# Performance work log

Measured on AMD Instinct MI355X. Metric: run time of the kernel, lower is better.

Reference implementation:

```python
import jax, jax.numpy as jnp
import numpy as np

N_FFT = 512
HOP = 128
WIN = 512
Q = 0.1
PCT_WIN = 31
FREQ_WIN = 5
TIME_WIN = 9
STRENGTH = 0.35
THRESH = 1.5
TEMP = 0.15
MIN_MASK = 0.08


def _hann_periodic(n):
    # matches torch.hann_window(n) (periodic)
    return (0.5 * (1.0 - jnp.cos(2.0 * jnp.pi * jnp.arange(n) / n))).astype(jnp.float32)


def _stft(x, window):
    # x: (B, L) -> complex (B, F, T); center=True, reflect pad
    pad = N_FFT // 2
    xp = jnp.pad(x, ((0, 0), (pad, pad)), mode='reflect')
    T = 1 + (xp.shape[-1] - N_FFT) // HOP
    idx = (jnp.arange(T) * HOP)[:, None] + jnp.arange(N_FFT)  # (T, n_fft)
    frames = xp[:, idx] * window  # (B, T, n_fft)
    return jnp.fft.rfft(frames, axis=-1).transpose(0, 2, 1)  # (B, F, T)


def _istft(spec, window, length):
    # spec: (B, F, T) complex -> (B, length)
    frames = jnp.fft.irfft(spec.transpose(0, 2, 1), n=N_FFT, axis=-1) * window  # (B,T,n_fft)
    B, T, _ = frames.shape
    total = N_FFT + HOP * (T - 1)
    idx = ((jnp.arange(T) * HOP)[:, None] + jnp.arange(N_FFT)).ravel()
    out = jnp.zeros((B, total), frames.dtype).at[:, idx].add(frames.reshape(B, -1))
    wsq = jnp.zeros((total,), frames.dtype).at[idx].add(
        jnp.broadcast_to(window ** 2, (T, N_FFT)).ravel())
    out = out / jnp.maximum(wsq, 1e-11)
    pad = N_FFT // 2
    return out[:, pad:pad + length]


def _rolling_quantile(mag):
    # mag: (B, F, T); replicate pad + sliding window of PCT_WIN along time
    p = PCT_WIN // 2
    padded = jnp.pad(mag, ((0, 0), (0, 0), (p, p)), mode='edge')
    T = mag.shape[-1]
    windows = jnp.stack([padded[..., i:i + T] for i in range(PCT_WIN)], axis=-1)  # (B,F,T,W)
    return jnp.quantile(windows, Q, axis=-1)


def _avg_pool(x, k, axis):
    # stride-1 avg pool with zero pad k//2, count_include_pad=True (torch default)
    if k <= 1:
        return x
    p = k // 2
    pads = [(0, 0)] * x.ndim
    pads[axis] = (p, p)
    xp = jnp.pad(x, pads)
    n = x.shape[axis]
    acc = 0.0
    for i in range(k):
        sl = [slice(None)] * x.ndim
        sl[axis] = slice(i, i + n)
        acc = acc + xp[tuple(sl)]
    return acc / k


def setup_inputs() -> dict:
    key = jax.random.key(0)
    k1, k2 = jax.random.split(key)
    B, L = 16, 160000
    noisy = jax.random.normal(k1, (B, L), dtype=jnp.float32)
    enhanced = jax.random.normal(k2, (B, L), dtype=jnp.float32)
    return {"noisy": noisy, "enhanced": enhanced}


def reference(noisy, enhanced):
    length = enhanced.shape[-1]
    window = _hann_periodic(WIN)
    e_spec = _stft(enhanced, window)
    n_spec = _stft(noisy, window)
    e_mag = jnp.maximum(jnp.abs(e_spec), 1e-6)
    n_mag = jnp.maximum(jnp.abs(n_spec), 1e-6)
    # mode == 'sg_input_floor': source is the noisy magnitude
    floor = _rolling_quantile(n_mag)
    floor = _avg_pool(floor, FREQ_WIN, axis=-2)
    floor = _avg_pool(floor, TIME_WIN, axis=-1)
    floor = jnp.maximum(floor, 1e-6)
    mask = jax.nn.sigmoid((e_mag - THRESH * floor) / (TEMP * floor + 1e-6))
    final_mask = MIN_MASK + (1.0 - MIN_MASK) * (1.0 - STRENGTH + STRENGTH * mask)
    phase = e_spec / jnp.maximum(jnp.abs(e_spec), 1e-12)  # unit-phase, = polar(1, angle)
    gated_spec = (e_mag * final_mask).astype(jnp.float32) * phase
    return _istft(gated_spec, window, length)
```

## Files before the change

### kernel.cpp

```cpp
#include <hip/hip_runtime.h>
#include <hip/hip_bf16.h>
#include <math.h>

#define BATCH 16
#define LEN   160000
#define NFFT  512
#define HOP   128
#define NT    1251
#define NF    257
#define PADC  256
#define TWO_PI 6.28318530717958647692f
#define P(i) ((i) + ((i) >> 5))
#define FBUF 528
#define GSTR 264

typedef unsigned int u32;
typedef unsigned short u16t;

__device__ __forceinline__ float rcpf(float x)  { return __builtin_amdgcn_rcpf(x); }
__device__ __forceinline__ float sqrtf_fast(float x) { return __builtin_amdgcn_sqrtf(x); }

__device__ __forceinline__ int reflect_idx(int j) {
    j = j < 0 ? -j : j;
    j = j >= LEN ? 2*LEN - 2 - j : j;
    return j;
}

__device__ __forceinline__ float hann(int n) {
    return 0.5f - 0.5f * __cosf(TWO_PI * (float)n * (1.0f / 512.0f));
}

__device__ __forceinline__ void hann8(int j, float wdv[8]) {
    float sth, cth;
    __sincosf((TWO_PI / 512.0f) * (float)j, &sth, &cth);
    const float K8 = 0.70710678118654752f;
    const float A = 0.5f * K8 * (cth - sth);
    const float B = 0.5f * K8 * (cth + sth);
    wdv[0] = 0.5f - 0.5f * cth;
    wdv[1] = 0.5f - A;
    wdv[2] = 0.5f + 0.5f * sth;
    wdv[3] = 0.5f + B;
    wdv[4] = 0.5f + 0.5f * cth;
    wdv[5] = 0.5f + A;
    wdv[6] = 0.5f - 0.5f * sth;
    wdv[7] = 0.5f - B;
}

__device__ __forceinline__ __hip_bfloat162 pack_bf2(float x, float y) {
    __hip_bfloat162 r; r.x = __float2bfloat16(x); r.y = __float2bfloat16(y); return r;
}
__device__ __forceinline__ float2 unpack_bf2(__hip_bfloat162 v) {
    return make_float2(__bfloat162float(v.x), __bfloat162float(v.y));
}

struct T4 { float m0, m1, m2, m3; };

__device__ __forceinline__ void ins(T4& a, float v) {
    const float x0 = fminf(a.m0, v);  const float c0 = fmaxf(a.m0, v);
    const float x1 = fminf(a.m1, c0); const float c1 = fmaxf(a.m1, c0);
    const float x2 = fminf(a.m2, c1); const float c2 = fmaxf(a.m2, c1);
    const float x3 = fminf(a.m3, c2);
    a.m0 = x0; a.m1 = x1; a.m2 = x2; a.m3 = x3;
}

__device__ __forceinline__ u32 pminP(u32 a, u32 b) {
    u32 d; asm("v_pk_min_u16 %0, %1, %2" : "=v"(d) : "v"(a), "v"(b)); return d;
}
__device__ __forceinline__ u32 pmaxP(u32 a, u32 b) {
    u32 d; asm("v_pk_max_u16 %0, %1, %2" : "=v"(d) : "v"(a), "v"(b)); return d;
}

struct PT4 { u32 m0, m1, m2, m3; };

__device__ __forceinline__ void insP(PT4& a, u32 v) {
    const u32 x0 = pminP(a.m0, v);  const u32 c0 = pmaxP(a.m0, v);
    const u32 x1 = pminP(a.m1, c0); const u32 c1 = pmaxP(a.m1, c0);
    const u32 x2 = pminP(a.m2, c1); const u32 c2 = pmaxP(a.m2, c1);
    const u32 x3 = pminP(a.m3, c2);
    a.m0 = x0; a.m1 = x1; a.m2 = x2; a.m3 = x3;
}

__device__ __forceinline__ PT4 sort4P(u32 a, u32 b, u32 c, u32 d) {
    const u32 x0 = pminP(a, b), x1 = pmaxP(a, b);
    const u32 x2 = pminP(c, d), x3 = pmaxP(c, d);
    const u32 y0 = pminP(x0, x2), y2 = pmaxP(x0, x2);
    const u32 y1 = pminP(x1, x3), y3 = pmaxP(x1, x3);
    PT4 r; r.m0 = y0; r.m1 = pminP(y1, y2); r.m2 = pmaxP(y1, y2); r.m3 = y3;
    return r;
}

__device__ __forceinline__ u32 merge4_m3P(const PT4& a, const PT4& b) {
    const u32 l0 = pminP(a.m0, b.m3);
    const u32 l1 = pminP(a.m1, b.m2);
    const u32 l2 = pminP(a.m2, b.m1);
    const u32 l3 = pminP(a.m3, b.m0);
    return pmaxP(pmaxP(l0, l1), pmaxP(l2, l3));
}

__device__ __forceinline__ void dft8(float vr[8], float vi[8], float sign) {
    const float K = 0.70710678118654752f;
    float ar=vr[0]+vr[4], ai=vi[0]+vi[4];
    float br=vr[0]-vr[4], bi=vi[0]-vi[4];
    float cr=vr[2]+vr[6], ci=vi[2]+vi[6];
    float dr=vr[2]-vr[6], di=vi[2]-vi[6];
    float er=vr[1]+vr[5], ei=vi[1]+vi[5];
    float fr=vr[1]-vr[5], fi=vi[1]-vi[5];
    float gr=vr[3]+vr[7], gi=vi[3]+vi[7];
    float hr=vr[3]-vr[7], hi=vi[3]-vi[7];
    const float W4dr = -sign*di, W4di = sign*dr;
    const float W4hr = -sign*hi, W4hi = sign*hr;
    const float E0r=ar+cr, E0i=ai+ci, E2r=ar-cr, E2i=ai-ci;
    const float E1r=br+W4dr, E1i=bi+W4di, E3r=br-W4dr, E3i=bi-W4di;
    const float O0r=er+gr, O0i=ei+gi, O2r=er-gr, O2i=ei-gi;
    const float O1r=fr+W4hr, O1i=fi+W4hi, O3r=fr-W4hr, O3i=fi-W4hi;
    const float T1r = K*(O1r - sign*O1i), T1i = K*(O1i + sign*O1r);
    const float T2r = -sign*O2i,          T2i = sign*O2r;
    const float T3r = K*(-O3r - sign*O3i), T3i = K*(-O3i + sign*O3r);
    vr[0]=E0r+O0r; vi[0]=E0i+O0i;  vr[4]=E0r-O0r; vi[4]=E0i-O0i;
    vr[1]=E1r+T1r; vi[1]=E1i+T1i;  vr[5]=E1r-T1r; vi[5]=E1i-T1i;
    vr[2]=E2r+T2r; vi[2]=E2i+T2i;  vr[6]=E2r-T2r; vi[6]=E2i-T2i;
    vr[3]=E3r+T3r; vi[3]=E3i+T3i;  vr[7]=E3r-T3r; vi[7]=E3i-T3i;
}

template<int NS>
__device__ __forceinline__ void fft_pass(float* R, float* I, int j, float sign) {
    float vr[8], vi[8];
    #pragma unroll
    for (int r = 0; r < 8; ++r) { vr[r] = R[P(j + 64*r)]; vi[r] = I[P(j + 64*r)]; }
    const float th = sign * (TWO_PI / (8.0f * (float)NS)) * (float)(j & (NS - 1));
    float w1r, w1i; __sincosf(th, &w1i, &w1r);
    float wr = w1r, wi = w1i;
    #pragma unroll
    for (int r = 1; r < 8; ++r) {
        const float tr = vr[r]*wr - vi[r]*wi;
        vi[r] = vr[r]*wi + vi[r]*wr; vr[r] = tr;
        const float nwr = wr*w1r - wi*w1i;
        wi = wr*w1i + wi*w1r; wr = nwr;
    }
    dft8(vr, vi, sign);
    const int base = ((j / NS) * (8 * NS)) + (j & (NS - 1));
    #pragma unroll
    for (int r = 0; r < 8; ++r) { R[P(base + r*NS)] = vr[r]; I[P(base + r*NS)] = vi[r]; }
}

__device__ __forceinline__ void fft_pass_last(const float* R, const float* I, int j,
                                              float sign, float vr[8], float vi[8]) {
    #pragma unroll
    for (int r = 0; r < 8; ++r) { vr[r] = R[P(j + 64*r)]; vi[r] = I[P(j + 64*r)]; }
    const float th = sign * (TWO_PI / 512.0f) * (float)j;
    float w1r, w1i; __sincosf(th, &w1i, &w1r);
    float wr = w1r, wi = w1i;
    #pragma unroll
    for (int r = 1; r < 8; ++r) {
        const float tr = vr[r]*wr - vi[r]*wi;
        vi[r] = vr[r]*wi + vi[r]*wr; vr[r] = tr;
        const float nwr = wr*w1r - wi*w1i;
        wi = wr*w1i + wi*w1r; wr = nwr;
    }
    dft8(vr, vi, sign);
}

__global__ __launch_bounds__(256, 6) void stft_kernel(const float* __restrict__ enh,
                                                      const float* __restrict__ noi,
                                                      __hip_bfloat162* __restrict__ e_spec,
                                                      __hip_bfloat16*  __restrict__ n_mag,
                                                      float* __restrict__ out) {
    __shared__ float Ar[4*FBUF], Ai[4*FBUF];
    const int tid = threadIdx.x;
    const int w = tid >> 6, j = tid & 63;
    const int tr_ = blockIdx.x * 4 + w;
    const bool live = tr_ < NT;
    const int t = live ? tr_ : NT - 1;
    const int b = blockIdx.y;
    float* ar = Ar + w*FBUF; float* ai = Ai + w*FBUF;

    {
        const int z = (blockIdx.x << 9) + (tid << 1);
        if (z < LEN) *reinterpret_cast<float2*>(out + (size_t)b * LEN + z) = make_float2(0.0f, 0.0f);
    }

    {
        const int sbase = t * HOP - PADC;
        float vr[8], vi[8];
        if (sbase >= 0 && sbase + NFFT <= LEN) {
            const float* __restrict__ pe = enh + b * LEN + sbase;
            const float* __restrict__ pn = noi + b * LEN + sbase;
            float wdv[8];
            hann8(j, wdv);
            #pragma unroll
            for (int r = 0; r < 8; ++r) {
                const int n = j + 64*r;
                vr[r] = pe[n] * wdv[r];
                vi[r] = pn[n] * wdv[r];
            }
        } else {
            const float* __restrict__ pe = enh + b * LEN;
            const float* __restrict__ pn = noi + b * LEN;
            #pragma unroll
            for (int r = 0; r < 8; ++r) {
                const int n = j + 64*r;
                const int idx = reflect_idx(sbase + n);
                const float wd = hann(n);
                vr[r] = pe[idx] * wd;
                vi[r] = pn[idx] * wd;
            }
        }
        dft8(vr, vi, -1.0f);
        #pragma unroll
        for (int r = 0; r < 8; ++r) { ar[P(8*j + r)] = vr[r]; ai[P(8*j + r)] = vi[r]; }
    }
    fft_pass<8>(ar, ai, j, -1.0f);
    float zr[8], zi[8];
    fft_pass_last(ar, ai, j, -1.0f, zr, zi);

    const int src = (64 - j) & 63;
    float pr[4], pi_[4];
    #pragma unroll
    for (int q = 4; q < 8; ++q) {
        pr[q-4]  = __shfl(zr[q], src);
        pi_[q-4] = __shfl(zi[q], src);
    }
    if (live) {
        const int obase = (b * NT + t) * NF;
        #pragma unroll
        for (int r = 0; r < 4; ++r) {
            const int kk = j + 64*r;
            const float yr = (j == 0) ? zr[(8 - r) & 7] : pr[3 - r];
            const float yi = (j == 0) ? zi[(8 - r) & 7] : pi_[3 - r];
            const float er = 0.5f*(zr[r] + yr), ei = 0.5f*(zi[r] - yi);
            const float nr = 0.5f*(zi[r] + yi), ni = 0.5f*(yr - zr[r]);
            e_spec[obase + kk] = pack_bf2(er, ei);
            n_mag[obase + kk] = __float2bfloat16(fmaxf(sqrtf_fast(nr*nr + ni*ni), 1e-6f));
        }
        if (j == 0) {
            e_spec[obase + 256] = pack_bf2(zr[4], 0.0f);
            n_mag[obase + 256] = __float2bfloat16(fmaxf(fabsf(zi[4]), 1e-6f));
        }
    }
}

template<bool CL>
__device__ __forceinline__ void phaseQP(const u16t* __restrict__ pbu,
                                        int t0, int f, float qv[16]) {
    u16t wlo[16];
    #pragma unroll
    for (int r = 0; r < 16; ++r) {
        int tr = t0 - 19 + r;
        if (CL) { tr = tr < 0 ? 0 : (tr > NT - 1 ? NT - 1 : tr); }
        wlo[r] = pbu[tr * NF + f];
    }
    PT4 S[8];
    S[7].m0 = (u32)wlo[7] | ((u32)wlo[15] << 16);
    S[7].m1 = S[7].m2 = S[7].m3 = 0xFFFFFFFFu;
    #pragma unroll
    for (int k = 6; k >= 0; --k) {
        S[k] = S[k+1];
        insP(S[k], (u32)wlo[k] | ((u32)wlo[k+8] << 16));
    }
    u16t ring[8];
    #pragma unroll
    for (int i = 0; i < 8; ++i) ring[i] = wlo[8 + i];
    PT4 Pp;
    {
        u32 Wt[4];
        #pragma unroll
        for (int r = 8; r < 12; ++r) {
            int tr = t0 - 19 + r + 8;
            if (CL) { tr = tr < 0 ? 0 : (tr > NT - 1 ? NT - 1 : tr); }
            const u16t hi = pbu[tr * NF + f];
            Wt[r - 8] = (u32)ring[r & 7] | ((u32)hi << 16);
            ring[r & 7] = hi;
        }
        Pp = sort4P(Wt[0], Wt[1], Wt[2], Wt[3]);
    }
    #pragma unroll
    for (int r = 12; r < 31; ++r) {
        int tr = t0 - 19 + r + 8;
        if (CL) { tr = tr < 0 ? 0 : (tr > NT - 1 ? NT - 1 : tr); }
        const u16t hi = pbu[tr * NF + f];
        insP(Pp, (u32)ring[r & 7] | ((u32)hi << 16));
        ring[r & 7] = hi;
    }
    {
        const u32 m = merge4_m3P(S[0], Pp);
        qv[0] = __uint_as_float(m << 16);
        qv[8] = __uint_as_float(m & 0xFFFF0000u);
    }
    #pragma unroll
    for (int k = 1; k < 8; ++k) {
        const int r = 30 + k;
        int tr = t0 - 19 + r + 8;
        if (CL) { tr = tr < 0 ? 0 : (tr > NT - 1 ? NT - 1 : tr); }
        const u16t hi = pbu[tr * NF + f];
        insP(Pp, (u32)ring[r & 7] | ((u32)hi << 16));
        ring[r & 7] = hi;
        const u32 m = merge4_m3P(S[k], Pp);
        qv[k]     = __uint_as_float(m << 16);
        qv[8 + k] = __uint_as_float(m & 0xFFFF0000u);
    }
}

__global__ __launch_bounds__(256, 4) void floor_mask_istft_kernel(
        const __hip_bfloat162* __restrict__ g,
        const __hip_bfloat16* __restrict__ n_mag,
        float* __restrict__ out) {
    __shared__ float smem[16 * GSTR];
    float* TPl = smem;
    float* gr = smem;
    float* gi = smem + 8 * GSTR;

    const int tid = threadIdx.x;
    const int w = tid >> 6, j = tid & 63;
    const int t0 = blockIdx.x * 8, b = blockIdx.y;
    const __hip_bfloat16* __restrict__ pb = n_mag + b * NT * NF;
    const u16t* __restrict__ pbu = (const u16t*)pb;
    const int f = tid;

    float qv[16];
    if (t0 >= 19 && t0 + 26 <= NT - 1) {
        phaseQP<false>(pbu, t0, f, qv);
    } else {
        phaseQP<true>(pbu, t0, f, qv);
        #pragma unroll
        for (int k = 0; k < 16; ++k) {
            const int tq = t0 - 4 + k;
            if (tq < 0 || tq >= NT) qv[k] = 0.0f;
        }
    }
    {
        float acc = 0.0f;
        #pragma unroll
        for (int k = 0; k < 9; ++k) acc += qv[k];
        #pragma unroll
        for (int to = 0; to < 8; ++to) {
            TPl[to * GSTR + f] = acc * (1.0f / 9.0f);
            if (to < 7) acc += qv[to + 9] - qv[to];
        }
    }
    if (tid < 16) {
        const int k = tid;
        T4 m; m.m0 = m.m1 = m.m2 = m.m3 = 3.4e38f;
        for (int dt = -15; dt <= 15; ++dt) {
            int tt = t0 - 4 + k + dt;
            tt = tt < 0 ? 0 : (tt > NT - 1 ? NT - 1 : tt);
            ins(m, __bfloat162float(pb[tt * NF + 256]));
        }
        float qk = m.m3;
        const int tq = t0 - 4 + k;
        if (tq < 0 || tq >= NT) qk = 0.0f;
        float acc = 0.0f;
        #pragma unroll
        for (int d = 0; d < 9; ++d) acc += __shfl(qk, k + d);
        if (tid < 8) TPl[tid * GSTR + 256] = acc * (1.0f / 9.0f);
    }
    __syncthreads();

    float fl[8];
    #pragma unroll
    for (int to = 0; to < 8; ++to) {
        float acc = 0.0f;
        #pragma unroll
        for (int df = -2; df <= 2; ++df) {
            const int ff = f + df;
            if (ff >= 0 && ff < NF) acc += TPl[to * GSTR + ff];
        }
        fl[to] = fmaxf(acc * (1.0f / 5.0f), 1e-6f);
    }
    float fl256 = 0.0f;
    if (tid < 8) {
        fl256 = fmaxf((TPl[tid * GSTR + 254] + TPl[tid * GSTR + 255] +
                       TPl[tid * GSTR + 256]) * (1.0f / 5.0f), 1e-6f);
    }
    __syncthreads();

    {
        #pragma unroll
        for (int ft = 0; ft < 8; ++ft) {
            const int t = t0 + ft;
            float grv = 0.0f, giv = 0.0f;
            if (t < NT) {
                const float flv = fl[ft];
                const float2 e2 = unpack_bf2(g[(b * NT + t) * NF + f]);
                const float a = sqrtf_fast(e2.x * e2.x + e2.y * e2.y);
                const float emag = fmaxf(a, 1e-6f);
                const float xarg = (emag - 1.5f * flv) * rcpf(0.15f * flv + 1e-6f);
                const float mask = rcpf(1.0f + __expf(-xarg));
                const float fm = 0.08f + 0.92f * (0.65f + 0.35f * mask);
                const float scale = emag * fm * rcpf(fmaxf(a, 1e-12f));
                grv = e2.x * scale; giv = e2.y * scale;
            }
            gr[ft * GSTR + f] = grv;
            gi[ft * GSTR + f] = giv;
        }
    }
    if (tid < 8) {
        const int ft = tid;
        const int t = t0 + ft;
        float grv = 0.0f, giv = 0.0f;
        if (t < NT) {
            const float flv = fl256;
            const float2 e2 = unpack_bf2(g[(b * NT + t) * NF + 256]);
            const float a = sqrtf_fast(e2.x * e2.x + e2.y * e2.y);
            const float emag = fmaxf(a, 1e-6f);
            const float xarg = (emag - 1.5f * flv) * rcpf(0.15f * flv + 1e-6f);
            const float mask = rcpf(1.0f + __expf(-xarg));
            const float fm = 0.08f + 0.92f * (0.65f + 0.35f * mask);
            const float scale = emag * fm * rcpf(fmaxf(a, 1e-12f));
            grv = e2.x * scale; giv = e2.y * scale;
        }
        gr[ft * GSTR + 256] = grv;
        gi[ft * GSTR + 256] = giv;
    }
    __syncthreads();

    float* g0r = gr + (2*w) * GSTR;      float* g0i = gi + (2*w) * GSTR;
    float* g1r = gr + (2*w + 1) * GSTR;  float* g1i = gi + (2*w + 1) * GSTR;
    float* ar = g0r;
    float* ai = g0i;

    {
        float vr[8], vi[8];
        #pragma unroll
        for (int r = 0; r < 8; ++r) {
            const int n = j + 64*r;
            float cr, ci;
            if (n <= 256) {
                cr = g0r[n] - g1i[n];
                ci = g0i[n] + g1r[n];
            } else {
                const int m = 512 - n;
                cr = g0r[m] + g1i[m];
                ci = g1r[m] - g0i[m];
            }
            vr[r] = cr; vi[r] = ci;
        }
        dft8(vr, vi, 1.0f);
        #pragma unroll
        for (int r = 0; r < 8; ++r) { ar[P(8*j + r)] = vr[r]; ai[P(8*j + r)] = vi[r]; }
    }
    fft_pass<8>(ar, ai, j, 1.0f);
    float xr[8], xi[8];
    fft_pass_last(ar, ai, j, 1.0f, xr, xi);

    {
        float wdv[8];
        hann8(j, wdv);
        #pragma unroll
        for (int r = 0; r < 8; ++r) {
            const int n = j + 64*r;
            const float wd = wdv[r] * (1.0f / 512.0f);
            ar[P(n)] = xr[r] * wd;
            ai[P(n)] = xi[r] * wd;
        }
    }
    __syncthreads();

    const int i0 = t0 << 7;
    if (t0 >= 3 && t0 + 10 <= NT - 1) {
        for (int s = tid; s < 1408; s += 256) {
            const int i = i0 + s;
            const int tl = (i - 384) >> 7;
            const int th = tl + 3;
            const int ca = tl > t0 ? tl : t0;
            const int cb = th < t0 + 7 ? th : t0 + 7;
            float acc = 0.0f;
            for (int t = ca; t <= cb; ++t) {
                const int ft = t - t0;
                const int n = i - (t << 7);
                acc += ((ft & 1) ? gi : gr)[(ft >> 1) * FBUF + P(n)];
            }
            const float v = acc * (2.0f / 3.0f);
            const int jj = i - PADC;
            if (tl >= t0 && th <= t0 + 7) out[b * LEN + jj] = v;
            else atomicAdd(out + b * LEN + jj, v);
        }
    } else {
        for (int s = tid; s < 1408; s += 256) {
            const int i = i0 + s;
            const int jj = i - PADC;
            if (jj < 0 || jj >= LEN) continue;
            const int tl = (i >= 384) ? ((i - 384) >> 7) : 0;
            int th = i >> 7; if (th > NT - 1) th = NT - 1;
            const int ca = tl > t0 ? tl : t0;
            const int cb = th < t0 + 7 ? th : t0 + 7;
            if (cb < ca) continue;
            float acc = 0.0f;
            for (int t = ca; t <= cb; ++t) {
                const int ft = t - t0;
                const int n = i - (t << 7);
                acc += ((ft & 1) ? gi : gr)[(ft >> 1) * FBUF + P(n)];
            }
            float winv;
            if (th - tl == 3) winv = (2.0f / 3.0f);
            else {
                float wacc = 0.0f;
                for (int t = tl; t <= th; ++t) {
                    const float wd = hann(i - (t << 7));
                    wacc += wd * wd;
                }
                winv = rcpf(fmaxf(wacc, 1e-11f));
            }
            const float v = acc * winv;
            if (tl >= t0 && th <= t0 + 7) out[b * LEN + jj] = v;
            else atomicAdd(out + b * LEN + jj, v);
        }
    }
}

extern "C" void kernel_launch(void* const* d_in, const int* in_sizes, int n_in,
                              void* d_out, int out_size, void* d_ws, size_t ws_size,
                              hipStream_t stream) {
    const float* noisy    = (const float*)d_in[0];
    const float* enhanced = (const float*)d_in[1];
    float* out = (float*)d_out;

    float* ws = (float*)d_ws;
    __hip_bfloat162* e_spec = (__hip_bfloat162*)ws;
    __hip_bfloat16* n_mag = (__hip_bfloat16*)(ws + 5144112);

    stft_kernel<<<dim3((NT + 3) / 4, BATCH), dim3(256), 0, stream>>>(enhanced, noisy, e_spec, n_mag, out);
    floor_mask_istft_kernel<<<dim3((NT + 7) / 8, BATCH), dim3(256), 0, stream>>>(e_spec, n_mag, out);
}
```

Measured before the change: 122.3 us.

## Widen floor/mask/iSTFT kernel to 16 frames per block with 512 threads

The fused floor/mask/iSTFT kernel now handles 16 time frames per block instead of 8, using 512 threads split into two halves. Each half computes 12 rolling-quantile values into shared memory, and the time-pool then reads them back. This amortizes the 31-wide quantile window halo and the iSTFT overlap edges (fewer atomicAdds) across more frames. In exchange it uses more shared memory per block, adds an extra barrier, and runs fewer, larger blocks, which changes occupancy.

```diff
diff --git a/kernel.cpp b/kernel.cpp
--- a/kernel.cpp
+++ b/kernel.cpp
@@ -240,104 +240,100 @@
 }
 
 template<bool CL>
-__device__ __forceinline__ void phaseQP(const u16t* __restrict__ pbu,
-                                        int t0, int f, float qv[16]) {
-    u16t wlo[16];
-    #pragma unroll
-    for (int r = 0; r < 16; ++r) {
-        int tr = t0 - 19 + r;
+__device__ __forceinline__ void phaseQ12(const u16t* __restrict__ pbu,
+                                         int base, int f, float qv[12]) {
+    u16t w0[12];
+    #pragma unroll
+    for (int r = 0; r < 12; ++r) {
+        int tr = base + r;
         if (CL) { tr = tr < 0 ? 0 : (tr > NT - 1 ? NT - 1 : tr); }
-        wlo[r] = pbu[tr * NF + f];
-    }
-    PT4 S[8];
-    S[7].m0 = (u32)wlo[7] | ((u32)wlo[15] << 16);
-    S[7].m1 = S[7].m2 = S[7].m3 = 0xFFFFFFFFu;
-    #pragma unroll
-    for (int k = 6; k >= 0; --k) {
+        w0[r] = pbu[tr * NF + f];
+    }
+    PT4 S[6];
+    S[5].m0 = (u32)w0[5] | ((u32)w0[11] << 16);
+    S[5].m1 = S[5].m2 = S[5].m3 = 0xFFFFFFFFu;
+    #pragma unroll
+    for (int k = 4; k >= 0; --k) {
         S[k] = S[k+1];
-        insP(S[k], (u32)wlo[k] | ((u32)wlo[k+8] << 16));
-    }
-    u16t ring[8];
-    #pragma unroll
-    for (int i = 0; i < 8; ++i) ring[i] = wlo[8 + i];
+        insP(S[k], (u32)w0[k] | ((u32)w0[k+6] << 16));
+    }
+    u16t ring[6];
+    #pragma unroll
+    for (int i = 0; i < 6; ++i) ring[i] = w0[6 + i];
     PT4 Pp;
     {
         u32 Wt[4];
         #pragma unroll
-        for (int r = 8; r < 12; ++r) {
-            int tr = t0 - 19 + r + 8;
+        for (int r = 6; r < 10; ++r) {
+            int tr = base + r + 6;
             if (CL) { tr = tr < 0 ? 0 : (tr > NT - 1 ? NT - 1 : tr); }
             const u16t hi = pbu[tr * NF + f];
-            Wt[r - 8] = (u32)ring[r & 7] | ((u32)hi << 16);
-            ring[r & 7] = hi;
+            Wt[r - 6] = (u32)ring[r % 6] | ((u32)hi << 16);
+            ring[r % 6] = hi;
         }
         Pp = sort4P(Wt[0], Wt[1], Wt[2], Wt[3]);
     }
     #pragma unroll
-    for (int r = 12; r < 31; ++r) {
-        int tr = t0 - 19 + r + 8;
+    for (int r = 10; r < 31; ++r) {
+        int tr = base + r + 6;
         if (CL) { tr = tr < 0 ? 0 : (tr > NT - 1 ? NT - 1 : tr); }
         const u16t hi = pbu[tr * NF + f];
-        insP(Pp, (u32)ring[r & 7] | ((u32)hi << 16));
-        ring[r & 7] = hi;
+        insP(Pp, (u32)ring[r % 6] | ((u32)hi << 16));
+        ring[r % 6] = hi;
     }
     {
         const u32 m = merge4_m3P(S[0], Pp);
         qv[0] = __uint_as_float(m << 16);
-        qv[8] = __uint_as_float(m & 0xFFFF0000u);
-    }
-    #pragma unroll
-    for (int k = 1; k < 8; ++k) {
+        qv[6] = __uint_as_float(m & 0xFFFF0000u);
+    }
+    #pragma unroll
+    for (int k = 1; k < 6; ++k) {
         const int r = 30 + k;
-        int tr = t0 - 19 + r + 8;
+        int tr = base + r + 6;
         if (CL) { tr = tr < 0 ? 0 : (tr > NT - 1 ? NT - 1 : tr); }
         const u16t hi = pbu[tr * NF + f];
-        insP(Pp, (u32)ring[r & 7] | ((u32)hi << 16));
-        ring[r & 7] = hi;
+        insP(Pp, (u32)ring[r % 6] | ((u32)hi << 16));
+        ring[r % 6] = hi;
         const u32 m = merge4_m3P(S[k], Pp);
         qv[k]     = __uint_as_float(m << 16);
-        qv[8 + k] = __uint_as_float(m & 0xFFFF0000u);
-    }
-}
-
-__global__ __launch_bounds__(256, 4) void floor_mask_istft_kernel(
+        qv[6 + k] = __uint_as_float(m & 0xFFFF0000u);
+    }
+}
+
+__global__ __launch_bounds__(512, 6) void floor_mask_istft_kernel(
         const __hip_bfloat162* __restrict__ g,
         const __hip_bfloat16* __restrict__ n_mag,
         float* __restrict__ out) {
-    __shared__ float smem[16 * GSTR];
-    float* TPl = smem;
+    __shared__ float smem[40 * GSTR];
+    float (*q)[GSTR] = reinterpret_cast<float (*)[GSTR]>(smem);
+    float* TPl = smem + 24 * GSTR;
     float* gr = smem;
-    float* gi = smem + 8 * GSTR;
+    float* gi = smem + 16 * GSTR;
 
     const int tid = threadIdx.x;
     const int w = tid >> 6, j = tid & 63;
-    const int t0 = blockIdx.x * 8, b = blockIdx.y;
+    const int h = tid >> 8, f = tid & 255;
+    const int t0 = blockIdx.x * 16, b = blockIdx.y;
     const __hip_bfloat16* __restrict__ pb = n_mag + b * NT * NF;
     const u16t* __restrict__ pbu = (const u16t*)pb;
-    const int f = tid;
-
-    float qv[16];
-    if (t0 >= 19 && t0 + 26 <= NT - 1) {
-        phaseQP<false>(pbu, t0, f, qv);
-    } else {
-        phaseQP<true>(pbu, t0, f, qv);
-        #pragma unroll
-        for (int k = 0; k < 16; ++k) {
-            const int tq = t0 - 4 + k;
-            if (tq < 0 || tq >= NT) qv[k] = 0.0f;
-        }
-    }
-    {
-        float acc = 0.0f;
-        #pragma unroll
-        for (int k = 0; k < 9; ++k) acc += qv[k];
-        #pragma unroll
-        for (int to = 0; to < 8; ++to) {
-            TPl[to * GSTR + f] = acc * (1.0f / 9.0f);
-            if (to < 7) acc += qv[to + 9] - qv[to];
-        }
-    }
-    if (tid < 16) {
+
+    {
+        float qv[12];
+        const int base = t0 - 19 + 12 * h;
+        if (t0 >= 19 && t0 + 34 <= NT - 1) {
+            phaseQ12<false>(pbu, base, f, qv);
+        } else {
+            phaseQ12<true>(pbu, base, f, qv);
+            #pragma unroll
+            for (int i = 0; i < 12; ++i) {
+                const int tq = t0 - 4 + 12 * h + i;
+                if (tq < 0 || tq >= NT) qv[i] = 0.0f;
+            }
+        }
+        #pragma unroll
+        for (int i = 0; i < 12; ++i) q[12 * h + i][f] = qv[i];
+    }
+    if (tid < 24) {
         const int k = tid;
         T4 m; m.m0 = m.m1 = m.m2 = m.m3 = 3.4e38f;
         for (int dt = -15; dt <= 15; ++dt) {
@@ -348,26 +344,45 @@
         float qk = m.m3;
         const int tq = t0 - 4 + k;
         if (tq < 0 || tq >= NT) qk = 0.0f;
+        q[k][256] = qk;
+    }
+    __syncthreads();
+
+    {
+        float qr[16];
+        #pragma unroll
+        for (int i = 0; i < 16; ++i) qr[i] = q[8 * h + i][f];
         float acc = 0.0f;
         #pragma unroll
-        for (int d = 0; d < 9; ++d) acc += __shfl(qk, k + d);
-        if (tid < 8) TPl[tid * GSTR + 256] = acc * (1.0f / 9.0f);
+        for (int i = 0; i < 9; ++i) acc += qr[i];
+        #pragma unroll
+        for (int ft_ = 0; ft_ < 8; ++ft_) {
+            TPl[(8 * h + ft_) * GSTR + f] = acc * (1.0f / 9.0f);
+            if (ft_ < 7) acc += qr[ft_ + 9] - qr[ft_];
+        }
+    }
+    if (tid < 16) {
+        float acc = 0.0f;
+        #pragma unroll
+        for (int d = 0; d < 9; ++d) acc += q[tid + d][256];
+        TPl[tid * GSTR + 256] = acc * (1.0f / 9.0f);
     }
     __syncthreads();
 
     float fl[8];
     #pragma unroll
-    for (int to = 0; to < 8; ++to) {
+    for (int ft_ = 0; ft_ < 8; ++ft_) {
+        const int row = 8 * h + ft_;
         float acc = 0.0f;
         #pragma unroll
         for (int df = -2; df <= 2; ++df) {
             const int ff = f + df;
-            if (ff >= 0 && ff < NF) acc += TPl[to * GSTR + ff];
-        }
-        fl[to] = fmaxf(acc * (1.0f / 5.0f), 1e-6f);
+            if (ff >= 0 && ff < NF) acc += TPl[row * GSTR + ff];
+        }
+        fl[ft_] = fmaxf(acc * (1.0f / 5.0f), 1e-6f);
     }
     float fl256 = 0.0f;
-    if (tid < 8) {
+    if (tid < 16) {
         fl256 = fmaxf((TPl[tid * GSTR + 254] + TPl[tid * GSTR + 255] +
                        TPl[tid * GSTR + 256]) * (1.0f / 5.0f), 1e-6f);
     }
@@ -375,11 +390,12 @@
 
     {
         #pragma unroll
-        for (int ft = 0; ft < 8; ++ft) {
+        for (int ft_ = 0; ft_ < 8; ++ft_) {
+            const int ft = 8 * h + ft_;
             const int t = t0 + ft;
             float grv = 0.0f, giv = 0.0f;
             if (t < NT) {
-                const float flv = fl[ft];
+                const float flv = fl[ft_];
                 const float2 e2 = unpack_bf2(g[(b * NT + t) * NF + f]);
                 const float a = sqrtf_fast(e2.x * e2.x + e2.y * e2.y);
                 const float emag = fmaxf(a, 1e-6f);
@@ -393,16 +409,15 @@
             gi[ft * GSTR + f] = giv;
         }
     }
-    if (tid < 8) {
+    if (tid < 16) {
         const int ft = tid;
         const int t = t0 + ft;
         float grv = 0.0f, giv = 0.0f;
         if (t < NT) {
-            const float flv = fl256;
             const float2 e2 = unpack_bf2(g[(b * NT + t) * NF + 256]);
             const float a = sqrtf_fast(e2.x * e2.x + e2.y * e2.y);
             const float emag = fmaxf(a, 1e-6f);
-            const float xarg = (emag - 1.5f * flv) * rcpf(0.15f * flv + 1e-6f);
+            const float xarg = (emag - 1.5f * fl256) * rcpf(0.15f * fl256 + 1e-6f);
             const float mask = rcpf(1.0f + __expf(-xarg));
             const float fm = 0.08f + 0.92f * (0.65f + 0.35f * mask);
             const float scale = emag * fm * rcpf(fmaxf(a, 1e-12f));
@@ -456,13 +471,13 @@
     __syncthreads();
 
     const int i0 = t0 << 7;
-    if (t0 >= 3 && t0 + 10 <= NT - 1) {
-        for (int s = tid; s < 1408; s += 256) {
+    if (t0 >= 3 && t0 + 18 <= NT - 1) {
+        for (int s = tid; s < 2432; s += 512) {
             const int i = i0 + s;
             const int tl = (i - 384) >> 7;
             const int th = tl + 3;
             const int ca = tl > t0 ? tl : t0;
-            const int cb = th < t0 + 7 ? th : t0 + 7;
+            const int cb = th < t0 + 15 ? th : t0 + 15;
             float acc = 0.0f;
             for (int t = ca; t <= cb; ++t) {
                 const int ft = t - t0;
@@ -471,18 +486,18 @@
             }
             const float v = acc * (2.0f / 3.0f);
             const int jj = i - PADC;
-            if (tl >= t0 && th <= t0 + 7) out[b * LEN + jj] = v;
+            if (tl >= t0 && th <= t0 + 15) out[b * LEN + jj] = v;
             else atomicAdd(out + b * LEN + jj, v);
         }
     } else {
-        for (int s = tid; s < 1408; s += 256) {
+        for (int s = tid; s < 2432; s += 512) {
             const int i = i0 + s;
             const int jj = i - PADC;
             if (jj < 0 || jj >= LEN) continue;
             const int tl = (i >= 384) ? ((i - 384) >> 7) : 0;
             int th = i >> 7; if (th > NT - 1) th = NT - 1;
             const int ca = tl > t0 ? tl : t0;
-            const int cb = th < t0 + 7 ? th : t0 + 7;
+            const int cb = th < t0 + 15 ? th : t0 + 15;
             if (cb < ca) continue;
             float acc = 0.0f;
             for (int t = ca; t <= cb; ++t) {
@@ -501,7 +516,7 @@
                 winv = rcpf(fmaxf(wacc, 1e-11f));
             }
             const float v = acc * winv;
-            if (tl >= t0 && th <= t0 + 7) out[b * LEN + jj] = v;
+            if (tl >= t0 && th <= t0 + 15) out[b * LEN + jj] = v;
             else atomicAdd(out + b * LEN + jj, v);
         }
     }
@@ -519,5 +534,5 @@
     __hip_bfloat16* n_mag = (__hip_bfloat16*)(ws + 5144112);
 
     stft_kernel<<<dim3((NT + 3) / 4, BATCH), dim3(256), 0, stream>>>(enhanced, noisy, e_spec, n_mag, out);
-    floor_mask_istft_kernel<<<dim3((NT + 7) / 8, BATCH), dim3(256), 0, stream>>>(e_spec, n_mag, out);
-}
+    floor_mask_istft_kernel<<<dim3((NT + 15) / 16, BATCH), dim3(512), 0, stream>>>(e_spec, n_mag, out);
+}
```

After: 120.6 us. No clear change (-1.4%).
